# Performance work log

Hardware: AMD Instinct MI355X
Metric: run time of the kernel (lower is better)

## Reference

```python
import jax, jax.numpy as jnp
import numpy as np

B, S, D, F, E = 4, 4096, 1024, 2048, 8


def setup_inputs() -> dict:
    key = jax.random.key(0)
    ks = jax.random.split(key, 8)
    x = jax.random.normal(ks[0], (B, S, D), dtype=jnp.float32)
    # router (nn.Linear(d_model, num_experts))
    Wr = jax.random.normal(ks[1], (D, E), dtype=jnp.float32) * 0.02
    br = jnp.zeros((E,), dtype=jnp.float32)
    # stacked per-expert MLP params: Linear(D,F) -> GELU -> Linear(F,D)
    W1 = jax.random.normal(ks[2], (E, D, F), dtype=jnp.float32) * (1.0 / np.sqrt(D))
    b1 = jnp.zeros((E, F), dtype=jnp.float32)
    W2 = jax.random.normal(ks[3], (E, F, D), dtype=jnp.float32) * (1.0 / np.sqrt(F))
    b2 = jnp.zeros((E, D), dtype=jnp.float32)
    return {"x": x, "Wr": Wr, "br": br, "W1": W1, "b1": b1, "W2": W2, "b2": b2}


def reference(x, Wr, br, W1, b1, W2, b2):
    # router: softmax over experts, top-1 selection
    logits = jnp.einsum("bsd,de->bse", x, Wr) + br          # [B,S,E]
    probs = jax.nn.softmax(logits, axis=-1)
    expert_weights = jnp.max(probs, axis=-1)                  # [B,S]
    expert_indices = jnp.argmax(probs, axis=-1)               # [B,S]

    num_experts = W1.shape[0]
    out = jnp.zeros_like(x)
    # loop over the small fixed set of experts (structurally distinct weights)
    for e in range(num_experts):
        h = jax.nn.gelu(jnp.einsum("bsd,df->bsf", x, W1[e]) + b1[e], approximate=False)
        y = jnp.einsum("bsf,fd->bsd", h, W2[e]) + b2[e]
        out = jnp.where((expert_indices == e)[..., None], y, out)

    return out * expert_weights[..., None]
```

## Files before the change

kernel.cpp:

```cpp
#include <hip/hip_runtime.h>
#include <hip/hip_bf16.h>


typedef __attribute__((ext_vector_type(8))) short short8;
typedef __attribute__((ext_vector_type(4))) float f32x4;

struct __align__(8) us4 { unsigned short x, y, z, w; };

__device__ __forceinline__ void gload16(const void* g, void* l) {
  __builtin_amdgcn_global_load_lds(
      (const __attribute__((address_space(1))) unsigned int*)g,
      (__attribute__((address_space(3))) unsigned int*)l, 16, 0, 0);
}

__device__ __forceinline__ unsigned short f2b(float f) {
  union { float f; unsigned u; } v; v.f = f;
  unsigned r = v.u + 0x7FFFu + ((v.u >> 16) & 1u);
  return (unsigned short)(r >> 16);
}

__global__ __launch_bounds__(256) void router_logits(
    const float* __restrict__ x, const float* __restrict__ Wr,
    const float* __restrict__ br, float* __restrict__ wts,
    int* __restrict__ eidx, unsigned short* __restrict__ xb)
{
  const int lane = threadIdx.x & 63;
  const int wid  = threadIdx.x >> 6;
  const int t = blockIdx.x * 4 + wid;

  const float4* x4 = (const float4*)(x + (size_t)t * 1024);
  float acc[8];
#pragma unroll
  for (int e = 0; e < 8; ++e) acc[e] = 0.f;
#pragma unroll
  for (int i = 0; i < 4; ++i) {
    float4 v = x4[lane + 64 * i];
    const int d = (lane + 64 * i) * 4;
    const float* wr = Wr + (size_t)d * 8;
    float xs[4] = {v.x, v.y, v.z, v.w};
    us4 o;
    o.x = f2b(v.x); o.y = f2b(v.y); o.z = f2b(v.z); o.w = f2b(v.w);
    *(us4*)(xb + (size_t)t * 1024 + (size_t)(lane + 64 * i) * 4) = o;
#pragma unroll
    for (int j = 0; j < 4; ++j) {
      float4 w0 = *(const float4*)(wr + j * 8);
      float4 w1 = *(const float4*)(wr + j * 8 + 4);
      acc[0] += xs[j] * w0.x; acc[1] += xs[j] * w0.y;
      acc[2] += xs[j] * w0.z; acc[3] += xs[j] * w0.w;
      acc[4] += xs[j] * w1.x; acc[5] += xs[j] * w1.y;
      acc[6] += xs[j] * w1.z; acc[7] += xs[j] * w1.w;
    }
  }
#pragma unroll
  for (int e = 0; e < 8; ++e) {
    float v = acc[e];
#pragma unroll
    for (int m = 32; m; m >>= 1) v += __shfl_xor(v, m, 64);
    acc[e] = v;
  }
  if (lane == 0) {
    float lg[8];
#pragma unroll
    for (int e = 0; e < 8; ++e) lg[e] = acc[e] + br[e];
    float mx = lg[0]; int bi = 0;
#pragma unroll
    for (int e = 1; e < 8; ++e) if (lg[e] > mx) { mx = lg[e]; bi = e; }
    float s = 0.f;
#pragma unroll
    for (int e = 0; e < 8; ++e) s += expf(lg[e] - mx);
    wts[t]  = 1.0f / s;
    eidx[t] = bi;
  }
}

__global__ __launch_bounds__(256) void bucketize(
    const int* __restrict__ eidx, int* __restrict__ cnt, int* __restrict__ list)
{
  __shared__ int lcnt[8], base[8];
  const int tid = threadIdx.x;
  if (tid < 8) lcnt[tid] = 0;
  __syncthreads();
  const int t = blockIdx.x * 256 + tid;
  const int e = eidx[t];
  const int lpos = atomicAdd(&lcnt[e], 1);
  __syncthreads();
  if (tid < 8) base[tid] = atomicAdd(&cnt[tid], lcnt[tid]);
  __syncthreads();
  list[e * 16384 + base[e] + lpos] = t;
}

__global__ __launch_bounds__(256) void transpose_cvt(
    const float* __restrict__ W, unsigned short* __restrict__ Wt, int K, int N)
{
  __shared__ float tl[64][65];
  const int e = blockIdx.z;
  const float* Wp = W + (size_t)e * K * N;
  unsigned short* Wtp = Wt + (size_t)e * K * N;
  const int k0 = blockIdx.y * 64, n0 = blockIdx.x * 64;
  const int r = threadIdx.x >> 4, c4 = (threadIdx.x & 15) * 4;
#pragma unroll
  for (int i = 0; i < 4; ++i) {
    float4 v = *(const float4*)(Wp + (size_t)(k0 + r + i * 16) * N + n0 + c4);
    tl[r + i * 16][c4 + 0] = v.x; tl[r + i * 16][c4 + 1] = v.y;
    tl[r + i * 16][c4 + 2] = v.z; tl[r + i * 16][c4 + 3] = v.w;
  }
  __syncthreads();
#pragma unroll
  for (int i = 0; i < 4; ++i) {
    const int n = r + i * 16;
    us4 o;
    o.x = f2b(tl[c4 + 0][n]); o.y = f2b(tl[c4 + 1][n]);
    o.z = f2b(tl[c4 + 2][n]); o.w = f2b(tl[c4 + 3][n]);
    *(us4*)(Wtp + (size_t)(n0 + n) * K + k0 + c4) = o;
  }
}

template <int K, int N, int EPI, int LOGNB>
__global__ __launch_bounds__(256, 4) void gemm_moe8(
    const unsigned short* __restrict__ A,
    const unsigned short* __restrict__ Bt,
    const float* __restrict__ bias,
    const int* __restrict__ cnt, const int* __restrict__ list,
    const float* __restrict__ wts, void* __restrict__ outp)
{
  constexpr int NT = K / 32;
  constexpr int NB = 1 << LOGNB;
  extern __shared__ char lds[];
  int*   tok_s = (int*)(lds + 49152);
  float* wt_s  = (float*)(lds + 49664);

  const int q = gridDim.x >> 3;
  const int p = ((int)blockIdx.x & 7) * q + ((int)blockIdx.x >> 3);
  int e = -1, pre = 0, cnte = 0, loc = p;
#pragma unroll
  for (int i = 0; i < 8; ++i) {
    const int c = cnt[i];
    const int bl = ((c + 127) >> 7) << LOGNB;
    if (e < 0) {
      if (loc < bl) { e = i; cnte = c; }
      else { loc -= bl; pre += c; }
    }
  }
  if (e < 0) return;
  const int row0 = (loc >> LOGNB) << 7;
  const int n0   = (loc & (NB - 1)) << 7;

  const int tid = threadIdx.x;
  const int lane = tid & 63, wid = tid >> 6;
  const int wr = wid >> 1, wc = wid & 1;
  const int l15 = lane & 15;

  if (tid < 128) {
    const int s = row0 + tid;
    if (s < cnte) {
      const int t = list[e * 16384 + s];
      tok_s[tid] = t;
      wt_s[tid]  = (EPI == 2) ? wts[t] : 0.f;
    } else { tok_s[tid] = 0; wt_s[tid] = 0.f; }
  }
  __syncthreads();

  const int srow = tid >> 2;
  const int gch  = ((tid & 3) ^ ((srow >> 1) & 3)) * 8;
  const unsigned short* aP[2];
  const unsigned short* bP[2];
#pragma unroll
  for (int k2 = 0; k2 < 2; ++k2) {
    const int row = k2 * 64 + srow;
    if (EPI == 1) aP[k2] = A + (size_t)tok_s[row] * K + gch;
    else          aP[k2] = A + (size_t)min(pre + row0 + row, 16383) * K + gch;
    bP[k2] = Bt + ((size_t)e * N + n0 + row) * K + gch;
  }

  const int xo = (((lane >> 4) ^ ((l15 >> 1) & 3)) << 4);
  const char* aB = lds + (size_t)(wr * 64 + l15) * 64 + xo;
  const char* bB = lds + 24576 + (size_t)(wc * 64 + l15) * 64 + xo;

  f32x4 acc[4][4];
#pragma unroll
  for (int m = 0; m < 4; ++m)
#pragma unroll
    for (int n = 0; n < 4; ++n) acc[m][n] = (f32x4){0.f, 0.f, 0.f, 0.f};

#define STG_A(S, T) do { _Pragma("unroll") \
    for (int k2 = 0; k2 < 2; ++k2) \
      gload16(aP[k2] + (size_t)(T) * 32, lds + (S) * 8192 + k2 * 4096 + (wid << 10)); \
  } while (0)
#define STG_B(S, T) do { _Pragma("unroll") \
    for (int k2 = 0; k2 < 2; ++k2) \
      gload16(bP[k2] + (size_t)(T) * 32, lds + 24576 + (S) * 8192 + k2 * 4096 + (wid << 10)); \
  } while (0)

#define TILE_BODY(T, SR, SS) do { \
    const int Ts_ = ((T) + 2 < NT) ? (T) + 2 : NT - 1;    \
    STG_A(SS, Ts_); \
    STG_B(SS, Ts_); \
    const char* aT = aB + (SR) * 8192; \
    const char* bT = bB + (SR) * 8192; \
    short8 aF[4], bF[4]; \
    _Pragma("unroll") \
    for (int m_ = 0; m_ < 4; ++m_) aF[m_] = *(const short8*)(aT + m_ * 1024); \
    _Pragma("unroll") \
    for (int n_ = 0; n_ < 4; ++n_) bF[n_] = *(const short8*)(bT + n_ * 1024); \
    __builtin_amdgcn_s_setprio(1); \
    _Pragma("unroll") \
    for (int m_ = 0; m_ < 4; ++m_) \
      _Pragma("unroll") \
      for (int n_ = 0; n_ < 4; ++n_) \
        acc[m_][n_] = __builtin_amdgcn_mfma_f32_16x16x32_bf16( \
            aF[m_], bF[n_], acc[m_][n_], 0, 0, 0); \
    __builtin_amdgcn_s_setprio(0); \
    asm volatile("s_waitcnt vmcnt(4)" ::: "memory");    \
    __builtin_amdgcn_s_barrier(); \
    asm volatile("" ::: "memory");    \
  } while (0)

  STG_A(0, 0); STG_B(0, 0);
  STG_A(1, 1); STG_B(1, 1);
  asm volatile("s_waitcnt vmcnt(4)" ::: "memory");
  __builtin_amdgcn_s_barrier();
  asm volatile("" ::: "memory");

#pragma unroll 1
  for (int T = 0; T < NT; T += 3) {
    TILE_BODY(T, 0, 2);
    if (T + 1 < NT) TILE_BODY(T + 1, 1, 0);
    if (T + 2 < NT) TILE_BODY(T + 2, 2, 1);
  }
#undef TILE_BODY
#undef STG_A
#undef STG_B
  asm volatile("s_waitcnt vmcnt(0)" ::: "memory");

  const int cRow0 = wr * 64 + ((lane >> 4) << 2);
  const int cColB = n0 + wc * 64 + l15;
  float bv[4];
#pragma unroll
  for (int nf = 0; nf < 4; ++nf) bv[nf] = bias[e * N + cColB + nf * 16];

  if (EPI == 1) {
    unsigned short* H = (unsigned short*)outp;
#pragma unroll
    for (int m = 0; m < 4; ++m)
#pragma unroll
      for (int r = 0; r < 4; ++r) {
        const int sl = cRow0 + m * 16 + r;
        if (row0 + sl < cnte) {
          const size_t rp = (size_t)(pre + row0 + sl) * N + cColB;
#pragma unroll
          for (int nf = 0; nf < 4; ++nf) {
            float v = acc[m][nf][r] + bv[nf];
            float u = 1.5957691216f * v * (1.0f + 0.044715f * v * v);
            float ex = __expf(u);
            float th = 1.0f - 2.0f / (ex + 1.0f);
            v = 0.5f * v * (1.0f + th);
            H[rp + nf * 16] = f2b(v);
          }
        }
      }
  } else {
    float* O = (float*)outp;
#pragma unroll
    for (int m = 0; m < 4; ++m)
#pragma unroll
      for (int r = 0; r < 4; ++r) {
        const int sl = cRow0 + m * 16 + r;
        if (row0 + sl < cnte) {
          const size_t rp = (size_t)tok_s[sl] * N + cColB;
          const float w = wt_s[sl];
#pragma unroll
          for (int nf = 0; nf < 4; ++nf)
            O[rp + nf * 16] = (acc[m][nf][r] + bv[nf]) * w;
        }
      }
  }
}

extern "C" void kernel_launch(void* const* d_in, const int* in_sizes, int n_in,
                              void* d_out, int out_size, void* d_ws, size_t ws_size,
                              hipStream_t stream) {
  const float* x  = (const float*)d_in[0];
  const float* Wr = (const float*)d_in[1];
  const float* br = (const float*)d_in[2];
  const float* W1 = (const float*)d_in[3];
  const float* b1 = (const float*)d_in[4];
  const float* W2 = (const float*)d_in[5];
  const float* b2 = (const float*)d_in[6];

  char* ws = (char*)d_ws;
  int*   cnt  = (int*)ws;
  float* wts  = (float*)(ws + 256);
  int*   eidx = (int*)(ws + 256 + 64 * 1024);
  int*   list = (int*)(ws + 256 + 128 * 1024);
  unsigned short* xb  = (unsigned short*)(ws + 1024 * 1024);
  unsigned short* w1t = xb  + (size_t)16384 * 1024;
  unsigned short* w2t = w1t + (size_t)8 * 2048 * 1024;
  unsigned short* h   = w2t + (size_t)8 * 1024 * 2048;

  constexpr int LDS_BYTES = 50176;
  hipFuncSetAttribute((const void*)gemm_moe8<1024, 2048, 1, 4>,
                      hipFuncAttributeMaxDynamicSharedMemorySize, LDS_BYTES);
  hipFuncSetAttribute((const void*)gemm_moe8<2048, 1024, 2, 3>,
                      hipFuncAttributeMaxDynamicSharedMemorySize, LDS_BYTES);

  hipMemsetAsync(cnt, 0, 32, stream);
  router_logits<<<dim3(4096), 256, 0, stream>>>(x, Wr, br, wts, eidx, xb);
  bucketize<<<dim3(64), 256, 0, stream>>>(eidx, cnt, list);
  transpose_cvt<<<dim3(32, 16, 8), 256, 0, stream>>>(W1, w1t, 1024, 2048);
  transpose_cvt<<<dim3(16, 32, 8), 256, 0, stream>>>(W2, w2t, 2048, 1024);
  gemm_moe8<1024, 2048, 1, 4><<<dim3(135 * 16), 256, LDS_BYTES, stream>>>(
      xb, w1t, b1, cnt, list, wts, (void*)h);
  gemm_moe8<2048, 1024, 2, 3><<<dim3(135 * 8), 256, LDS_BYTES, stream>>>(
      h, w2t, b2, cnt, list, wts, d_out);
}
```

Measured before the change: 319.0 us.

## Load MoE GEMM A operand directly into registers, keep B in LDS

The expert GEMM no longer stages the gathered activation tile (A) through shared memory. Each wave now reads its A fragments straight from global memory into registers, double-buffered one tile ahead. The freed LDS gives B a four-stage ring, the main loop is unrolled by four, and the launch-bounds occupancy hint drops from 4 to 3 blocks per CU to leave room for the extra registers. The aim is to cut LDS traffic and the A staging writes. In exchange, the two waves that share the same A rows both fetch them from global memory, and A latency is only hidden behind one tile of MFMA work.

```diff
diff --git a/kernel.cpp b/kernel.cpp
--- a/kernel.cpp
+++ b/kernel.cpp
@@ -116,7 +116,7 @@
 }
 
 template <int K, int N, int EPI, int LOGNB>
-__global__ __launch_bounds__(256, 4) void gemm_moe8(
+__global__ __launch_bounds__(256, 3) void gemm_moe8(
     const unsigned short* __restrict__ A,
     const unsigned short* __restrict__ Bt,
     const float* __restrict__ bias,
@@ -126,8 +126,8 @@
   constexpr int NT = K / 32;
   constexpr int NB = 1 << LOGNB;
   extern __shared__ char lds[];
-  int*   tok_s = (int*)(lds + 49152);
-  float* wt_s  = (float*)(lds + 49664);
+  int*   tok_s = (int*)(lds + 32768);
+  float* wt_s  = (float*)(lds + 33280);
 
   const int q = gridDim.x >> 3;
   const int p = ((int)blockIdx.x & 7) * q + ((int)blockIdx.x >> 3);
@@ -148,7 +148,7 @@
   const int tid = threadIdx.x;
   const int lane = tid & 63, wid = tid >> 6;
   const int wr = wid >> 1, wc = wid & 1;
-  const int l15 = lane & 15;
+  const int l15 = lane & 15, hi = lane >> 4;
 
   if (tid < 128) {
     const int s = row0 + tid;
@@ -160,21 +160,23 @@
   }
   __syncthreads();
 
+  const unsigned short* aRP[4];
+#pragma unroll
+  for (int m = 0; m < 4; ++m) {
+    const int row = wr * 64 + m * 16 + l15;
+    if (EPI == 1) aRP[m] = A + (size_t)tok_s[row] * K + hi * 8;
+    else          aRP[m] = A + (size_t)min(pre + row0 + row, 16383) * K + hi * 8;
+  }
+
   const int srow = tid >> 2;
   const int gch  = ((tid & 3) ^ ((srow >> 1) & 3)) * 8;
-  const unsigned short* aP[2];
   const unsigned short* bP[2];
 #pragma unroll
-  for (int k2 = 0; k2 < 2; ++k2) {
-    const int row = k2 * 64 + srow;
-    if (EPI == 1) aP[k2] = A + (size_t)tok_s[row] * K + gch;
-    else          aP[k2] = A + (size_t)min(pre + row0 + row, 16383) * K + gch;
-    bP[k2] = Bt + ((size_t)e * N + n0 + row) * K + gch;
-  }
-
-  const int xo = (((lane >> 4) ^ ((l15 >> 1) & 3)) << 4);
-  const char* aB = lds + (size_t)(wr * 64 + l15) * 64 + xo;
-  const char* bB = lds + 24576 + (size_t)(wc * 64 + l15) * 64 + xo;
+  for (int k2 = 0; k2 < 2; ++k2)
+    bP[k2] = Bt + ((size_t)e * N + n0 + k2 * 64 + srow) * K + gch;
+
+  const int xo = ((hi ^ ((l15 >> 1) & 3)) << 4);
+  const char* bB = lds + (size_t)(wc * 64 + l15) * 64 + xo;
 
   f32x4 acc[4][4];
 #pragma unroll
@@ -182,24 +184,22 @@
 #pragma unroll
     for (int n = 0; n < 4; ++n) acc[m][n] = (f32x4){0.f, 0.f, 0.f, 0.f};
 
-#define STG_A(S, T) do { _Pragma("unroll") \
-    for (int k2 = 0; k2 < 2; ++k2) \
-      gload16(aP[k2] + (size_t)(T) * 32, lds + (S) * 8192 + k2 * 4096 + (wid << 10)); \
-  } while (0)
 #define STG_B(S, T) do { _Pragma("unroll") \
     for (int k2 = 0; k2 < 2; ++k2) \
-      gload16(bP[k2] + (size_t)(T) * 32, lds + 24576 + (S) * 8192 + k2 * 4096 + (wid << 10)); \
+      gload16(bP[k2] + (size_t)(T) * 32, lds + (S) * 8192 + k2 * 4096 + (wid << 10)); \
   } while (0)
-
-#define TILE_BODY(T, SR, SS) do { \
-    const int Ts_ = ((T) + 2 < NT) ? (T) + 2 : NT - 1;    \
-    STG_A(SS, Ts_); \
+#define PREF_A(DST, T) do { _Pragma("unroll") \
+    for (int m_ = 0; m_ < 4; ++m_) \
+      DST[m_] = *(const short8*)(aRP[m_] + (size_t)(T) * 32); \
+  } while (0)
+
+#define TILE_BODY(T, SR, SS, AC, AN) do { \
+    const int Tn_ = ((T) + 1 < NT) ? (T) + 1 : NT - 1; \
+    const int Ts_ = ((T) + 2 < NT) ? (T) + 2 : NT - 1; \
+    PREF_A(AN, Tn_); \
     STG_B(SS, Ts_); \
-    const char* aT = aB + (SR) * 8192; \
     const char* bT = bB + (SR) * 8192; \
-    short8 aF[4], bF[4]; \
-    _Pragma("unroll") \
-    for (int m_ = 0; m_ < 4; ++m_) aF[m_] = *(const short8*)(aT + m_ * 1024); \
+    short8 bF[4]; \
     _Pragma("unroll") \
     for (int n_ = 0; n_ < 4; ++n_) bF[n_] = *(const short8*)(bT + n_ * 1024); \
     __builtin_amdgcn_s_setprio(1); \
@@ -208,31 +208,34 @@
       _Pragma("unroll") \
       for (int n_ = 0; n_ < 4; ++n_) \
         acc[m_][n_] = __builtin_amdgcn_mfma_f32_16x16x32_bf16( \
-            aF[m_], bF[n_], acc[m_][n_], 0, 0, 0); \
+            AC[m_], bF[n_], acc[m_][n_], 0, 0, 0); \
     __builtin_amdgcn_s_setprio(0); \
-    asm volatile("s_waitcnt vmcnt(4)" ::: "memory");    \
+    asm volatile("s_waitcnt vmcnt(2)" ::: "memory");    \
     __builtin_amdgcn_s_barrier(); \
-    asm volatile("" ::: "memory");    \
+    asm volatile("" ::: "memory"); \
   } while (0)
 
-  STG_A(0, 0); STG_B(0, 0);
-  STG_A(1, 1); STG_B(1, 1);
-  asm volatile("s_waitcnt vmcnt(4)" ::: "memory");
+  short8 aX[4], aY[4];
+  PREF_A(aX, 0);
+  STG_B(0, 0);
+  STG_B(1, 1);
+  asm volatile("s_waitcnt vmcnt(2)" ::: "memory");
   __builtin_amdgcn_s_barrier();
   asm volatile("" ::: "memory");
 
 #pragma unroll 1
-  for (int T = 0; T < NT; T += 3) {
-    TILE_BODY(T, 0, 2);
-    if (T + 1 < NT) TILE_BODY(T + 1, 1, 0);
-    if (T + 2 < NT) TILE_BODY(T + 2, 2, 1);
+  for (int T = 0; T < NT; T += 4) {
+    TILE_BODY(T,     0, 2, aX, aY);
+    TILE_BODY(T + 1, 1, 3, aY, aX);
+    TILE_BODY(T + 2, 2, 0, aX, aY);
+    TILE_BODY(T + 3, 3, 1, aY, aX);
   }
 #undef TILE_BODY
-#undef STG_A
 #undef STG_B
+#undef PREF_A
   asm volatile("s_waitcnt vmcnt(0)" ::: "memory");
 
-  const int cRow0 = wr * 64 + ((lane >> 4) << 2);
+  const int cRow0 = wr * 64 + (hi << 2);
   const int cColB = n0 + wc * 64 + l15;
   float bv[4];
 #pragma unroll
@@ -297,7 +300,7 @@
   unsigned short* w2t = w1t + (size_t)8 * 2048 * 1024;
   unsigned short* h   = w2t + (size_t)8 * 1024 * 2048;
 
-  constexpr int LDS_BYTES = 50176;
+  constexpr int LDS_BYTES = 33792;
   hipFuncSetAttribute((const void*)gemm_moe8<1024, 2048, 1, 4>,
                       hipFuncAttributeMaxDynamicSharedMemorySize, LDS_BYTES);
   hipFuncSetAttribute((const void*)gemm_moe8<2048, 1024, 2, 3>,
```

Result: slower. 472.7 us (+48.2%).

## Fold weight transposes into router and first GEMM launches to overlap work

Applied to the files above, without the earlier changes.

The W1 transpose-and-convert now runs as extra blocks of the router kernel (renamed prep). The W2 transpose runs as extra trailing blocks of the first expert GEMM launch. This removes two separate kernel launches and lets the memory-bound weight conversion overlap with router and GEMM compute. In exchange, the GEMM launch has a larger grid, and the transpose blocks compete for CUs and reuse the GEMM's large dynamic LDS allocation, which may reduce occupancy for those blocks.

```diff
diff --git a/kernel.cpp b/kernel.cpp
--- a/kernel.cpp
+++ b/kernel.cpp
@@ -19,14 +19,47 @@
   return (unsigned short)(r >> 16);
 }
 
-__global__ __launch_bounds__(256) void router_logits(
+__global__ __launch_bounds__(256) void prep(
     const float* __restrict__ x, const float* __restrict__ Wr,
     const float* __restrict__ br, float* __restrict__ wts,
-    int* __restrict__ eidx, unsigned short* __restrict__ xb)
+    int* __restrict__ eidx, unsigned short* __restrict__ xb,
+    const float* __restrict__ W1, unsigned short* __restrict__ w1t)
 {
-  const int lane = threadIdx.x & 63;
-  const int wid  = threadIdx.x >> 6;
-  const int t = blockIdx.x * 4 + wid;
+  const int bid = blockIdx.x;
+  const int tid = threadIdx.x;
+
+  if (bid >= 4096) {
+    __shared__ float tl[64][65];
+    const int lb = bid - 4096;
+    const int ez = lb >> 9;
+    const int rem = lb & 511;
+    const int by = rem >> 5;
+    const int bx = rem & 31;
+    const float* Wp = W1 + (size_t)ez * 1024 * 2048;
+    unsigned short* Wtp = w1t + (size_t)ez * 1024 * 2048;
+    const int k0 = by * 64, n0 = bx * 64;
+    const int r = tid >> 4, c4 = (tid & 15) * 4;
+#pragma unroll
+    for (int i = 0; i < 4; ++i) {
+      float4 v = *(const float4*)(Wp + (size_t)(k0 + r + i * 16) * 2048 + n0 + c4);
+      tl[r + i * 16][c4 + 0] = v.x; tl[r + i * 16][c4 + 1] = v.y;
+      tl[r + i * 16][c4 + 2] = v.z; tl[r + i * 16][c4 + 3] = v.w;
+    }
+    __syncthreads();
+#pragma unroll
+    for (int i = 0; i < 4; ++i) {
+      const int n = r + i * 16;
+      us4 o;
+      o.x = f2b(tl[c4 + 0][n]); o.y = f2b(tl[c4 + 1][n]);
+      o.z = f2b(tl[c4 + 2][n]); o.w = f2b(tl[c4 + 3][n]);
+      *(us4*)(Wtp + (size_t)(n0 + n) * 1024 + k0 + c4) = o;
+    }
+    return;
+  }
+
+  const int lane = tid & 63;
+  const int wid  = tid >> 6;
+  const int t = bid * 4 + wid;
 
   const float4* x4 = (const float4*)(x + (size_t)t * 1024);
   float acc[8];
@@ -89,39 +122,14 @@
   list[e * 16384 + base[e] + lpos] = t;
 }
 
-__global__ __launch_bounds__(256) void transpose_cvt(
-    const float* __restrict__ W, unsigned short* __restrict__ Wt, int K, int N)
-{
-  __shared__ float tl[64][65];
-  const int e = blockIdx.z;
-  const float* Wp = W + (size_t)e * K * N;
-  unsigned short* Wtp = Wt + (size_t)e * K * N;
-  const int k0 = blockIdx.y * 64, n0 = blockIdx.x * 64;
-  const int r = threadIdx.x >> 4, c4 = (threadIdx.x & 15) * 4;
-#pragma unroll
-  for (int i = 0; i < 4; ++i) {
-    float4 v = *(const float4*)(Wp + (size_t)(k0 + r + i * 16) * N + n0 + c4);
-    tl[r + i * 16][c4 + 0] = v.x; tl[r + i * 16][c4 + 1] = v.y;
-    tl[r + i * 16][c4 + 2] = v.z; tl[r + i * 16][c4 + 3] = v.w;
-  }
-  __syncthreads();
-#pragma unroll
-  for (int i = 0; i < 4; ++i) {
-    const int n = r + i * 16;
-    us4 o;
-    o.x = f2b(tl[c4 + 0][n]); o.y = f2b(tl[c4 + 1][n]);
-    o.z = f2b(tl[c4 + 2][n]); o.w = f2b(tl[c4 + 3][n]);
-    *(us4*)(Wtp + (size_t)(n0 + n) * K + k0 + c4) = o;
-  }
-}
-
-template <int K, int N, int EPI, int LOGNB>
+template <int K, int N, int EPI, int LOGNB, int TFUSE>
 __global__ __launch_bounds__(256, 4) void gemm_moe8(
     const unsigned short* __restrict__ A,
     const unsigned short* __restrict__ Bt,
     const float* __restrict__ bias,
     const int* __restrict__ cnt, const int* __restrict__ list,
-    const float* __restrict__ wts, void* __restrict__ outp)
+    const float* __restrict__ wts, void* __restrict__ outp,
+    int nG, const float* __restrict__ Wsrc, unsigned short* __restrict__ Wdst)
 {
   constexpr int NT = K / 32;
   constexpr int NB = 1 << LOGNB;
@@ -129,8 +137,40 @@
   int*   tok_s = (int*)(lds + 49152);
   float* wt_s  = (float*)(lds + 49664);
 
-  const int q = gridDim.x >> 3;
-  const int p = ((int)blockIdx.x & 7) * q + ((int)blockIdx.x >> 3);
+  const int bid = blockIdx.x;
+  const int tid = threadIdx.x;
+
+  if (TFUSE && bid >= nG) {
+    float* tl = (float*)lds;
+    const int lb = bid - nG;
+    const int ez = lb >> 9;
+    const int rem = lb & 511;
+    const int by = rem >> 4;
+    const int bx = rem & 15;
+    const float* Wp = Wsrc + (size_t)ez * 2048 * 1024;
+    unsigned short* Wtp = Wdst + (size_t)ez * 2048 * 1024;
+    const int k0 = by * 64, nn0 = bx * 64;
+    const int r = tid >> 4, c4 = (tid & 15) * 4;
+#pragma unroll
+    for (int i = 0; i < 4; ++i) {
+      float4 v = *(const float4*)(Wp + (size_t)(k0 + r + i * 16) * 1024 + nn0 + c4);
+      tl[(r + i * 16) * 65 + c4 + 0] = v.x; tl[(r + i * 16) * 65 + c4 + 1] = v.y;
+      tl[(r + i * 16) * 65 + c4 + 2] = v.z; tl[(r + i * 16) * 65 + c4 + 3] = v.w;
+    }
+    __syncthreads();
+#pragma unroll
+    for (int i = 0; i < 4; ++i) {
+      const int n = r + i * 16;
+      us4 o;
+      o.x = f2b(tl[(c4 + 0) * 65 + n]); o.y = f2b(tl[(c4 + 1) * 65 + n]);
+      o.z = f2b(tl[(c4 + 2) * 65 + n]); o.w = f2b(tl[(c4 + 3) * 65 + n]);
+      *(us4*)(Wtp + (size_t)(nn0 + n) * 2048 + k0 + c4) = o;
+    }
+    return;
+  }
+
+  const int q = nG >> 3;
+  const int p = (bid & 7) * q + (bid >> 3);
   int e = -1, pre = 0, cnte = 0, loc = p;
 #pragma unroll
   for (int i = 0; i < 8; ++i) {
@@ -145,7 +185,6 @@
   const int row0 = (loc >> LOGNB) << 7;
   const int n0   = (loc & (NB - 1)) << 7;
 
-  const int tid = threadIdx.x;
   const int lane = tid & 63, wid = tid >> 6;
   const int wr = wid >> 1, wc = wid & 1;
   const int l15 = lane & 15;
@@ -298,18 +337,16 @@
   unsigned short* h   = w2t + (size_t)8 * 1024 * 2048;
 
   constexpr int LDS_BYTES = 50176;
-  hipFuncSetAttribute((const void*)gemm_moe8<1024, 2048, 1, 4>,
+  hipFuncSetAttribute((const void*)gemm_moe8<1024, 2048, 1, 4, 1>,
                       hipFuncAttributeMaxDynamicSharedMemorySize, LDS_BYTES);
-  hipFuncSetAttribute((const void*)gemm_moe8<2048, 1024, 2, 3>,
+  hipFuncSetAttribute((const void*)gemm_moe8<2048, 1024, 2, 3, 0>,
                       hipFuncAttributeMaxDynamicSharedMemorySize, LDS_BYTES);
 
   hipMemsetAsync(cnt, 0, 32, stream);
-  router_logits<<<dim3(4096), 256, 0, stream>>>(x, Wr, br, wts, eidx, xb);
+  prep<<<dim3(8192), 256, 0, stream>>>(x, Wr, br, wts, eidx, xb, W1, w1t);
   bucketize<<<dim3(64), 256, 0, stream>>>(eidx, cnt, list);
-  transpose_cvt<<<dim3(32, 16, 8), 256, 0, stream>>>(W1, w1t, 1024, 2048);
-  transpose_cvt<<<dim3(16, 32, 8), 256, 0, stream>>>(W2, w2t, 2048, 1024);
-  gemm_moe8<1024, 2048, 1, 4><<<dim3(135 * 16), 256, LDS_BYTES, stream>>>(
-      xb, w1t, b1, cnt, list, wts, (void*)h);
-  gemm_moe8<2048, 1024, 2, 3><<<dim3(135 * 8), 256, LDS_BYTES, stream>>>(
-      h, w2t, b2, cnt, list, wts, d_out);
-}
+  gemm_moe8<1024, 2048, 1, 4, 1><<<dim3(135 * 16 + 4096), 256, LDS_BYTES, stream>>>(
+      xb, w1t, b1, cnt, list, wts, (void*)h, 135 * 16, W2, w2t);
+  gemm_moe8<2048, 1024, 2, 3, 0><<<dim3(135 * 8), 256, LDS_BYTES, stream>>>(
+      h, w2t, b2, cnt, list, wts, d_out, 135 * 8, nullptr, nullptr);
+}
```

After: 302.0 us. 1.06x faster.
